# Kernel tuning notes

Hardware: AMD Instinct MI355X
Metric: run time of the kernel (lower is better)

## Reference

```python
import jax, jax.numpy as jnp
import numpy as np

SEQ, B, XD = 2048, 4, 16
D, NH, DFF, L, M = 256, 8, 512, 2, 1024
DH = D // NH
NEG_INF = -1e9  # finite stand-in for -inf (same softmax result, grad-safe)


def setup_inputs() -> dict:
    key = jax.random.key(0)
    ks = iter(jax.random.split(key, 40))

    def w(shape, s=0.02):
        return jax.random.normal(next(ks), shape, dtype=jnp.float32) * s

    return {
        "x": jax.random.normal(next(ks), (SEQ, B, XD), dtype=jnp.float32),
        "y": jax.random.normal(next(ks), (SEQ, B), dtype=jnp.float32),
        "single_eval_pos": M,
        "xenc_w": w((D, XD)), "xenc_b": w((D,)),
        "yenc_w": w((D, 1)), "yenc_b": w((D,)),
        "in_proj_w": w((L, 3 * D, D)), "in_proj_b": w((L, 3 * D)),
        "out_proj_w": w((L, D, D)), "out_proj_b": w((L, D)),
        "ln1_g": jnp.ones((L, D), jnp.float32), "ln1_b": jnp.zeros((L, D), jnp.float32),
        "lin1_w": w((L, DFF, D)), "lin1_b": w((L, DFF)),
        "lin2_w": w((L, D, DFF)), "lin2_b": w((L, D)),
        "ln2_g": jnp.ones((L, D), jnp.float32), "ln2_b": jnp.zeros((L, D), jnp.float32),
        "head_w1": w((DFF, D)), "head_b1": w((DFF,)),
        "head_w2": w((1, DFF)), "head_b2": w((1,)),
    }


def _layer_norm(x, g, b, eps=1e-5):
    mu = jnp.mean(x, axis=-1, keepdims=True)
    var = jnp.var(x, axis=-1, keepdims=True)
    return (x - mu) * jax.lax.rsqrt(var + eps) * g + b


def _forward(x, y, M_, p):
    seq, batch = y.shape
    x_src = x @ p["xenc_w"].T + p["xenc_b"]                     # [seq, b, D]
    y_src = y[..., None] @ p["yenc_w"].T + p["yenc_b"]           # [seq, b, D]
    tokens = jnp.concatenate([x_src[:M_] + y_src[:M_], x_src[M_:]], axis=0)

    # prefix-block + diagonal mask: keep (j < M) or (i == j)
    i = jnp.arange(seq)
    keep = (i[None, :] < M_) | (i[:, None] == i[None, :])
    mask = jnp.where(keep, 0.0, NEG_INF).astype(tokens.dtype)    # [seq, seq]

    h = tokens
    for l in range(p["in_proj_w"].shape[0]):
        qkv = h @ p["in_proj_w"][l].T + p["in_proj_b"][l]        # [seq, b, 3D]
        q, k, v = jnp.split(qkv, 3, axis=-1)
        to_heads = lambda t: t.reshape(seq, batch, NH, DH).transpose(1, 2, 0, 3)
        q, k, v = to_heads(q), to_heads(k), to_heads(v)          # [b, h, s, dh]
        scores = jnp.einsum("bhqd,bhkd->bhqk", q, k) / np.float32(np.sqrt(DH)) + mask
        attn = jax.nn.softmax(scores, axis=-1)
        o = jnp.einsum("bhqk,bhkd->bhqd", attn, v)
        o = o.transpose(2, 0, 1, 3).reshape(seq, batch, D)
        o = o @ p["out_proj_w"][l].T + p["out_proj_b"][l]
        h = _layer_norm(h + o, p["ln1_g"][l], p["ln1_b"][l])      # post-norm
        ff = jax.nn.gelu(h @ p["lin1_w"][l].T + p["lin1_b"][l], approximate=False)
        ff = ff @ p["lin2_w"][l].T + p["lin2_b"][l]
        h = _layer_norm(h + ff, p["ln2_g"][l], p["ln2_b"][l])

    q_out = h[M_:]                                               # [seq-M, b, D]
    hid = jax.nn.gelu(q_out @ p["head_w1"].T + p["head_b1"], approximate=False)
    return hid @ p["head_w2"].T + p["head_b2"]                   # [seq-M, b, 1]


def reference(x, y, single_eval_pos, xenc_w, xenc_b, yenc_w, yenc_b,
              in_proj_w, in_proj_b, out_proj_w, out_proj_b,
              ln1_g, ln1_b, lin1_w, lin1_b, lin2_w, lin2_b, ln2_g, ln2_b,
              head_w1, head_b1, head_w2, head_b2):
    p = dict(xenc_w=xenc_w, xenc_b=xenc_b, yenc_w=yenc_w, yenc_b=yenc_b,
             in_proj_w=in_proj_w, in_proj_b=in_proj_b,
             out_proj_w=out_proj_w, out_proj_b=out_proj_b,
             ln1_g=ln1_g, ln1_b=ln1_b, lin1_w=lin1_w, lin1_b=lin1_b,
             lin2_w=lin2_w, lin2_b=lin2_b, ln2_g=ln2_g, ln2_b=ln2_b,
             head_w1=head_w1, head_b1=head_b1, head_w2=head_w2, head_b2=head_b2)
    return _forward(x, y, int(single_eval_pos), p)
```

## Files before the change

kernel.cpp:

```cpp
#include <hip/hip_runtime.h>
#include <hip/hip_bf16.h>
#include <math.h>

#define SEQ    2048
#define BATCH  4
#define XDIM   16
#define DMODEL 256
#define NHEAD  8
#define DH     32
#define DFF    512
#define NLAYER 2
#define MPOS   1024
#define ROWS   (SEQ*BATCH)

#define ATT_SCALE 0.17677669529663687f

typedef __attribute__((ext_vector_type(8))) short bf16x8;
typedef __attribute__((ext_vector_type(4))) float f32x4;

__device__ __forceinline__ float gelu_exact(float x) {
    return 0.5f * x * (1.0f + erff(x * 0.70710678118654752f));
}
__device__ __forceinline__ short f2bf(float f) {
    unsigned int u = __float_as_uint(f);
    u += 0x7FFFu + ((u >> 16) & 1u);
    return (short)(u >> 16);
}
__device__ __forceinline__ float bf2f(unsigned short u) {
    return __uint_as_float(((unsigned int)u) << 16);
}
__device__ __forceinline__ void gload16(const unsigned short* g, unsigned short* l) {
    __builtin_amdgcn_global_load_lds(
        (const __attribute__((address_space(1))) unsigned int*)g,
        (__attribute__((address_space(3))) unsigned int*)l, 16, 0, 0);
}
#define VMWAIT(N) asm volatile("s_waitcnt vmcnt(" #N ")" ::: "memory")
__device__ __forceinline__ void pipe_barrier() {
    __builtin_amdgcn_sched_barrier(0);
    __builtin_amdgcn_s_barrier();
    __builtin_amdgcn_sched_barrier(0);
}

__global__ __launch_bounds__(256) void encode_cast(
    const float* __restrict__ x, const float* __restrict__ y,
    const float* __restrict__ xw, const float* __restrict__ xb,
    const float* __restrict__ yw, const float* __restrict__ yb,
    float* __restrict__ h, unsigned short* __restrict__ hb,
    const float* __restrict__ s0, const float* __restrict__ s1,
    const float* __restrict__ s2, const float* __restrict__ s3,
    const float* __restrict__ s4,
    unsigned short* __restrict__ d0, unsigned short* __restrict__ d1,
    unsigned short* __restrict__ d2, unsigned short* __restrict__ d3,
    unsigned short* __restrict__ d4)
{
    if (blockIdx.x < ROWS/4) {
        int g = blockIdx.x;
        int d = threadIdx.x;
        __shared__ float xs[4][XDIM];
        __shared__ float ys[4];
        if (d < 64) xs[d>>4][d&15] = x[(size_t)(g*4 + (d>>4))*XDIM + (d&15)];
        if (d < 4)  ys[d] = y[g*4 + d];
        __syncthreads();
        float wreg[XDIM];
        #pragma unroll
        for (int k = 0; k < XDIM; ++k) wreg[k] = xw[d*XDIM + k];
        const float xbv = xb[d], ywv = yw[d], ybv = yb[d];
        const bool train = (g < MPOS);
        #pragma unroll
        for (int r = 0; r < 4; ++r) {
            int row = g*4 + r;
            float acc = xbv;
            #pragma unroll
            for (int k = 0; k < XDIM; ++k) acc = fmaf(xs[r][k], wreg[k], acc);
            if (train) acc += ys[r]*ywv + ybv;
            h[(size_t)row*DMODEL + d]  = acc;
            hb[(size_t)row*DMODEL + d] = (unsigned short)f2bf(acc);
        }
        return;
    }
    int i = (blockIdx.x - ROWS/4)*256 + threadIdx.x;
    if (i >= 147456) return;
    const float* s; unsigned short* d; int off;
    if      (i <  49152) { s = s0; d = d0; off = i; }
    else if (i <  65536) { s = s1; d = d1; off = i - 49152; }
    else if (i <  98304) { s = s2; d = d2; off = i - 65536; }
    else if (i < 131072) { s = s3; d = d3; off = i - 98304; }
    else                 { s = s4; d = d4; off = i - 131072; }
    float4 a = *(const float4*)(s + (size_t)off*8);
    float4 c = *(const float4*)(s + (size_t)off*8 + 4);
    ushort4 u0, u1;
    u0.x=(unsigned short)f2bf(a.x); u0.y=(unsigned short)f2bf(a.y);
    u0.z=(unsigned short)f2bf(a.z); u0.w=(unsigned short)f2bf(a.w);
    u1.x=(unsigned short)f2bf(c.x); u1.y=(unsigned short)f2bf(c.y);
    u1.z=(unsigned short)f2bf(c.z); u1.w=(unsigned short)f2bf(c.w);
    *(ushort4*)(d + (size_t)off*8)     = u0;
    *(ushort4*)(d + (size_t)off*8 + 4) = u1;
}

__global__ __launch_bounds__(256) void gemm_qkv(
    const unsigned short* __restrict__ A, const unsigned short* __restrict__ B,
    const float* __restrict__ bias,
    unsigned short* __restrict__ Qg, unsigned short* __restrict__ Kg,
    unsigned short* __restrict__ Vg, int K)
{
    __shared__ unsigned short As[2][128][64];
    __shared__ unsigned short Bs[2][64][64];
    int tid  = threadIdx.x;
    int w    = tid >> 6, lane = tid & 63;
    int col  = lane & 15, quad = lane >> 4;
    int u    = blockIdx.x >> 3, xcd = blockIdx.x & 7;
    int by   = xcd*8 + u/12, bx = u%12;
    int m0   = by * 128, n0 = bx * 64;
    int l8   = lane >> 3;
    int c8s  = (((lane & 7) ^ l8) * 8);

    f32x4 acc[2][4];
    #pragma unroll
    for (int i = 0; i < 2; ++i)
        #pragma unroll
        for (int j = 0; j < 4; ++j) acc[i][j] = (f32x4){0.f,0.f,0.f,0.f};

    const unsigned short* ga = A + (size_t)(m0 + w*32 + l8)*K + c8s;
    const unsigned short* gb = B + (size_t)(n0 + w*16 + l8)*K + c8s;
    const int NS = K / 64;

    #pragma unroll
    for (int t = 0; t < 4; ++t) gload16(ga + (size_t)(t*8)*K, &As[0][w*32 + t*8][0]);
    #pragma unroll
    for (int t = 0; t < 2; ++t) gload16(gb + (size_t)(t*8)*K, &Bs[0][w*16 + t*8][0]);

    for (int s = 0; s < NS; ++s) {
        VMWAIT(0);
        pipe_barrier();
        if (s + 1 < NS) {
            int k2 = (s + 1) * 64;
            int nb = (s + 1) & 1;
            #pragma unroll
            for (int t = 0; t < 4; ++t) gload16(ga + k2 + (size_t)(t*8)*K, &As[nb][w*32 + t*8][0]);
            #pragma unroll
            for (int t = 0; t < 2; ++t) gload16(gb + k2 + (size_t)(t*8)*K, &Bs[nb][w*16 + t*8][0]);
        }
        int cur = s & 1;
        #pragma unroll
        for (int kk = 0; kk < 2; ++kk) {
            const int so = (((kk*4 + quad) ^ (col & 7)) * 8);
            bf16x8 af[2], bfr[4];
            #pragma unroll
            for (int i = 0; i < 2; ++i) af[i]  = *(const bf16x8*)&As[cur][w*32 + i*16 + col][so];
            #pragma unroll
            for (int j = 0; j < 4; ++j) bfr[j] = *(const bf16x8*)&Bs[cur][j*16 + col][so];
            #pragma unroll
            for (int i = 0; i < 2; ++i)
                #pragma unroll
                for (int j = 0; j < 4; ++j)
                    acc[i][j] = __builtin_amdgcn_mfma_f32_16x16x32_bf16(bfr[j], af[i], acc[i][j], 0, 0, 0);
        }
    }

    int region = n0 >> 8;
    if (region < 2) {
        #pragma unroll
        for (int i = 0; i < 2; ++i) {
            int m = m0 + w*32 + i*16 + col;
            int s = m >> 2, bidx = m & 3;
            #pragma unroll
            for (int j = 0; j < 4; ++j) {
                int ng = n0 + j*16 + quad*4;
                float4 bi = *(const float4*)&bias[ng];
                ushort4 uu;
                uu.x=(unsigned short)f2bf(acc[i][j][0] + bi.x);
                uu.y=(unsigned short)f2bf(acc[i][j][1] + bi.y);
                uu.z=(unsigned short)f2bf(acc[i][j][2] + bi.z);
                uu.w=(unsigned short)f2bf(acc[i][j][3] + bi.w);
                int np = ng - (region << 8);
                int hh = np >> 5, d = np & 31;
                int bh = bidx*NHEAD + hh;
                if (region == 0)
                    *(ushort4*)(Qg + ((size_t)(bh*SEQ + s))*DH + d) = uu;
                else
                    *(ushort4*)(Kg + ((size_t)(bh*SEQ + s))*DH + d) = uu;
            }
        }
    } else {
        __syncthreads();
        unsigned short* T3 = (unsigned short*)As;
        #pragma unroll
        for (int i = 0; i < 2; ++i) {
            int mi = w*32 + i*16 + col;
            int ss = mi >> 2, bidx = mi & 3;
            #pragma unroll
            for (int j = 0; j < 4; ++j) {
                int ni = j*16 + quad*4;
                float4 bi = *(const float4*)&bias[n0 + ni];
                T3[((ni    )*4 + bidx)*32 + ss] = (unsigned short)f2bf(acc[i][j][0] + bi.x);
                T3[((ni + 1)*4 + bidx)*32 + ss] = (unsigned short)f2bf(acc[i][j][1] + bi.y);
                T3[((ni + 2)*4 + bidx)*32 + ss] = (unsigned short)f2bf(acc[i][j][2] + bi.z);
                T3[((ni + 3)*4 + bidx)*32 + ss] = (unsigned short)f2bf(acc[i][j][3] + bi.w);
            }
        }
        __syncthreads();
        int sBase = m0 >> 2;
        #pragma unroll
        for (int r = 0; r < 4; ++r) {
            int chunk = tid + 256*r;
            int l = chunk >> 2, p = chunk & 3;
            int d = l & 31, hh_l = (l >> 5) & 1, bidx = l >> 6;
            int ni = hh_l*32 + d;
            int hh = ((n0 & 255) + ni) >> 5;
            int bh = bidx*NHEAD + hh;
            uint4 val = *(const uint4*)&T3[(ni*4 + bidx)*32 + p*8];
            *(uint4*)(Vg + ((size_t)(bh*DH + d))*SEQ + sBase + p*8) = val;
        }
    }
}

__global__ __launch_bounds__(256) void attn_mfma(
    const unsigned short* __restrict__ Qg,
    const unsigned short* __restrict__ Kg,
    const unsigned short* __restrict__ Vg,
    unsigned short* __restrict__ o)
{
    const int id  = blockIdx.x;
    const int sl  = id >> 3;
    const int bh  = (id & 7) * 4 + (sl >> 4);
    const int qt2 = sl & 15;
    const int h   = bh & 7;
    const int b   = bh >> 3;
    const int q0A = qt2 * 64;
    const int q0B = MPOS + qt2 * 64;
    const int tid  = threadIdx.x;
    const int w    = tid >> 6;
    const int lane = tid & 63;
    const int col  = lane & 15;
    const int quad = lane >> 4;

    __shared__ unsigned short Kt[2][128][40];
    __shared__ unsigned short Vt[2][32][136];
    __shared__ unsigned short PtA[4][16][136];
    __shared__ unsigned short PtB[4][16][136];

    const int qA = q0A + 16*w + col;
    const int qB = q0B + 16*w + col;
    bf16x8 qfA = *(const bf16x8*)(Qg + ((size_t)(bh*SEQ + qA))*DH + quad*8);
    bf16x8 qfB = *(const bf16x8*)(Qg + ((size_t)(bh*SEQ + qB))*DH + quad*8);

    f32x4 O0A = {0.f,0.f,0.f,0.f}, O1A = {0.f,0.f,0.f,0.f};
    f32x4 O0B = {0.f,0.f,0.f,0.f}, O1B = {0.f,0.f,0.f,0.f};
    float lsumA = 0.f, lsumB = 0.f;

    const int kRow = tid >> 2, kCh = (tid & 3) * 8;
    const int vD   = tid >> 3, vCh = (tid & 7) * 8;

    uint4 kreg0 = *(const uint4*)(Kg + ((size_t)(bh*SEQ + kRow     ))*DH + kCh);
    uint4 kreg1 = *(const uint4*)(Kg + ((size_t)(bh*SEQ + kRow + 64))*DH + kCh);
    uint4 vreg0 = *(const uint4*)(Vg + ((size_t)(bh*DH + vD))*SEQ + vCh);
    uint4 vreg1 = *(const uint4*)(Vg + ((size_t)(bh*DH + vD))*SEQ + vCh + 64);

    for (int kt = 0; kt < 8; ++kt) {
        const int p = kt & 1;
        *(uint4*)&Kt[p][kRow     ][kCh] = kreg0;
        *(uint4*)&Kt[p][kRow + 64][kCh] = kreg1;
        *(uint4*)&Vt[p][vD][vCh     ]   = vreg0;
        *(uint4*)&Vt[p][vD][vCh + 64]   = vreg1;
        __syncthreads();
        if (kt < 7) {
            int kn = (kt + 1) * 128;
            kreg0 = *(const uint4*)(Kg + ((size_t)(bh*SEQ + kn + kRow     ))*DH + kCh);
            kreg1 = *(const uint4*)(Kg + ((size_t)(bh*SEQ + kn + kRow + 64))*DH + kCh);
            vreg0 = *(const uint4*)(Vg + ((size_t)(bh*DH + vD))*SEQ + kn + vCh);
            vreg1 = *(const uint4*)(Vg + ((size_t)(bh*DH + vD))*SEQ + kn + vCh + 64);
        } else {
            kreg0 = *(const uint4*)(Kg + ((size_t)(bh*SEQ + q0B + kRow))*DH + kCh);
            vreg0 = *(const uint4*)(Vg + ((size_t)(bh*DH + vD))*SEQ + q0B + vCh);
        }

        #pragma unroll
        for (int mt = 0; mt < 8; ++mt) {
            bf16x8 kf = *(const bf16x8*)&Kt[p][mt*16 + col][quad*8];
            f32x4 stA = {0.f,0.f,0.f,0.f};
            stA = __builtin_amdgcn_mfma_f32_16x16x32_bf16(kf, qfA, stA, 0, 0, 0);
            ushort4 pwA;
            #pragma unroll
            for (int i = 0; i < 4; ++i) {
                float pv = __expf(stA[i]*ATT_SCALE);
                unsigned short us = (unsigned short)f2bf(pv);
                ((unsigned short*)&pwA)[i] = us;
                lsumA += bf2f(us);
            }
            *(ushort4*)&PtA[w][col][mt*16 + quad*4] = pwA;

            f32x4 stB = {0.f,0.f,0.f,0.f};
            stB = __builtin_amdgcn_mfma_f32_16x16x32_bf16(kf, qfB, stB, 0, 0, 0);
            ushort4 pwB;
            #pragma unroll
            for (int i = 0; i < 4; ++i) {
                float pv = __expf(stB[i]*ATT_SCALE);
                unsigned short us = (unsigned short)f2bf(pv);
                ((unsigned short*)&pwB)[i] = us;
                lsumB += bf2f(us);
            }
            *(ushort4*)&PtB[w][col][mt*16 + quad*4] = pwB;
        }
        #pragma unroll
        for (int c = 0; c < 4; ++c) {
            bf16x8 v0 = *(const bf16x8*)&Vt[p][col     ][c*32 + quad*8];
            bf16x8 v1 = *(const bf16x8*)&Vt[p][col + 16][c*32 + quad*8];
            bf16x8 pfA = *(const bf16x8*)&PtA[w][col][c*32 + quad*8];
            O0A = __builtin_amdgcn_mfma_f32_16x16x32_bf16(v0, pfA, O0A, 0, 0, 0);
            O1A = __builtin_amdgcn_mfma_f32_16x16x32_bf16(v1, pfA, O1A, 0, 0, 0);
            bf16x8 pfB = *(const bf16x8*)&PtB[w][col][c*32 + quad*8];
            O0B = __builtin_amdgcn_mfma_f32_16x16x32_bf16(v0, pfB, O0B, 0, 0, 0);
            O1B = __builtin_amdgcn_mfma_f32_16x16x32_bf16(v1, pfB, O1B, 0, 0, 0);
        }
    }

    *(uint4*)&Kt[0][kRow][kCh] = kreg0;
    *(uint4*)&Vt[0][vD][vCh]   = vreg0;
    __syncthreads();
    #pragma unroll
    for (int mt = 0; mt < 4; ++mt) {
        bf16x8 kf = *(const bf16x8*)&Kt[0][mt*16 + col][quad*8];
        f32x4 stB = {0.f,0.f,0.f,0.f};
        stB = __builtin_amdgcn_mfma_f32_16x16x32_bf16(kf, qfB, stB, 0, 0, 0);
        ushort4 pwB;
        #pragma unroll
        for (int i = 0; i < 4; ++i) {
            float pv = __expf(stB[i]*ATT_SCALE);
            if (mt*16 + quad*4 + i != 16*w + col) pv = 0.f;
            unsigned short us = (unsigned short)f2bf(pv);
            ((unsigned short*)&pwB)[i] = us;
            lsumB += bf2f(us);
        }
        *(ushort4*)&PtB[w][col][mt*16 + quad*4] = pwB;
    }
    #pragma unroll
    for (int c = 0; c < 2; ++c) {
        bf16x8 v0 = *(const bf16x8*)&Vt[0][col     ][c*32 + quad*8];
        bf16x8 v1 = *(const bf16x8*)&Vt[0][col + 16][c*32 + quad*8];
        bf16x8 pfB = *(const bf16x8*)&PtB[w][col][c*32 + quad*8];
        O0B = __builtin_amdgcn_mfma_f32_16x16x32_bf16(v0, pfB, O0B, 0, 0, 0);
        O1B = __builtin_amdgcn_mfma_f32_16x16x32_bf16(v1, pfB, O1B, 0, 0, 0);
    }

    lsumA += __shfl_xor(lsumA, 16, 64); lsumA += __shfl_xor(lsumA, 32, 64);
    lsumB += __shfl_xor(lsumB, 16, 64); lsumB += __shfl_xor(lsumB, 32, 64);
    float invA = 1.0f / lsumA, invB = 1.0f / lsumB;
    ushort4 u0, u1;
    #pragma unroll
    for (int i = 0; i < 4; ++i) {
        ((unsigned short*)&u0)[i] = (unsigned short)f2bf(O0A[i]*invA);
        ((unsigned short*)&u1)[i] = (unsigned short)f2bf(O1A[i]*invA);
    }
    unsigned short* opA = o + ((size_t)(qA*BATCH + b))*DMODEL + h*DH;
    *(ushort4*)(opA + quad*4)      = u0;
    *(ushort4*)(opA + 16 + quad*4) = u1;
    #pragma unroll
    for (int i = 0; i < 4; ++i) {
        ((unsigned short*)&u0)[i] = (unsigned short)f2bf(O0B[i]*invB);
        ((unsigned short*)&u1)[i] = (unsigned short)f2bf(O1B[i]*invB);
    }
    unsigned short* opB = o + ((size_t)(qB*BATCH + b))*DMODEL + h*DH;
    *(ushort4*)(opB + quad*4)      = u0;
    *(ushort4*)(opB + 16 + quad*4) = u1;
}

__global__ __launch_bounds__(256) void mlp_fused(
    const unsigned short* __restrict__ attb,
    const unsigned short* __restrict__ Wout, const float* __restrict__ ob,
    const float* __restrict__ g1, const float* __restrict__ be1,
    const unsigned short* __restrict__ W1, const float* __restrict__ fb1,
    const unsigned short* __restrict__ W2, const float* __restrict__ fb2,
    const float* __restrict__ g2, const float* __restrict__ be2,
    float* __restrict__ h, unsigned short* __restrict__ hb,
    const unsigned short* __restrict__ Wh1, const float* __restrict__ hb1,
    const float* __restrict__ hw2, const float* __restrict__ hb2,
    float* __restrict__ out, int doHead)
{
    __shared__ unsigned short Bs[3][256][64];
    __shared__ __align__(16) unsigned char smem_u[33280];
    __shared__ unsigned short Ht[2][16][264];
    __shared__ float sP[2][4][16], qP[2][4][16];

    typedef unsigned short AsT[2][16][64];
    AsT* As = reinterpret_cast<AsT*>(smem_u);
    typedef unsigned short PtT[16][520];
    PtT* Pt = reinterpret_cast<PtT*>(smem_u);

    const int tid  = threadIdx.x;
    const int w    = tid >> 6;
    const int lane = tid & 63;
    const int col  = lane & 15;
    const int quad = lane >> 4;
    const int l8   = lane >> 3;
    const int c8s  = (((lane & 7) ^ l8) * 8);
    const int bid  = blockIdx.x;
    const int m0a  = bid * 16;
    const int m0b  = 4096 + bid * 16;
    const int ma   = m0a + col;
    const int mb   = m0b + col;

    float resid[2][4][4];

    {
        f32x4 acc[2][4];
        #pragma unroll
        for (int g = 0; g < 2; ++g)
            #pragma unroll
            for (int j = 0; j < 4; ++j) acc[g][j] = (f32x4){0.f,0.f,0.f,0.f};

        const int gr = w >> 1;
        const unsigned short* gaw = attb + (size_t)((gr ? m0b : m0a) + (w&1)*8 + l8)*DMODEL + c8s;
        const unsigned short* gb  = Wout + (size_t)(w*64 + l8)*DMODEL + c8s;
        const int NS = DMODEL / 64;

        #pragma unroll
        for (int pb = 0; pb < 2; ++pb) {
            int k = pb * 64;
            gload16(gaw + k, &As[pb][gr][(w&1)*8][0]);
            #pragma unroll
            for (int t = 0; t < 8; ++t)
                gload16(gb + k + (size_t)(t*8)*DMODEL, &Bs[pb][w*64 + t*8][0]);
        }
        int bcur = 0;
        for (int s = 0; s < NS; ++s) {
            if (s == NS - 1) { VMWAIT(0); } else { VMWAIT(9); }
            pipe_barrier();
            if (s + 2 < NS) {
                int bpre = bcur + 2; if (bpre >= 3) bpre -= 3;
                int k2 = (s + 2) * 64;
                gload16(gaw + k2, &As[bpre][gr][(w&1)*8][0]);
                #pragma unroll
                for (int t = 0; t < 8; ++t)
                    gload16(gb + k2 + (size_t)(t*8)*DMODEL, &Bs[bpre][w*64 + t*8][0]);
            }
            #pragma unroll
            for (int kk = 0; kk < 2; ++kk) {
                const int so = (((kk*4 + quad) ^ (col & 7)) * 8);
                bf16x8 af0 = *(const bf16x8*)&As[bcur][0][col][so];
                bf16x8 af1 = *(const bf16x8*)&As[bcur][1][col][so];
                #pragma unroll
                for (int j = 0; j < 4; ++j) {
                    bf16x8 bfr = *(const bf16x8*)&Bs[bcur][w*64 + j*16 + col][so];
                    acc[0][j] = __builtin_amdgcn_mfma_f32_16x16x32_bf16(bfr, af0, acc[0][j], 0, 0, 0);
                    acc[1][j] = __builtin_amdgcn_mfma_f32_16x16x32_bf16(bfr, af1, acc[1][j], 0, 0, 0);
                }
            }
            bcur = (bcur == 2) ? 0 : bcur + 1;
        }

        float ssum[2] = {0.f, 0.f}, qsum[2] = {0.f, 0.f};
        #pragma unroll
        for (int g = 0; g < 2; ++g) {
            int m = g ? mb : ma;
            #pragma unroll
            for (int j = 0; j < 4; ++j) {
                int n = w*64 + j*16 + quad*4;
                float4 bi = *(const float4*)&ob[n];
                float4 hv = *(const float4*)&h[(size_t)m*DMODEL + n];
                #pragma unroll
                for (int i = 0; i < 4; ++i) {
                    float val = acc[g][j][i] + ((const float*)&bi)[i] + ((const float*)&hv)[i];
                    resid[g][j][i] = val;
                    ssum[g] += val; qsum[g] += val*val;
                }
            }
        }
        #pragma unroll
        for (int g = 0; g < 2; ++g) {
            ssum[g] += __shfl_xor(ssum[g], 16, 64); ssum[g] += __shfl_xor(ssum[g], 32, 64);
            qsum[g] += __shfl_xor(qsum[g], 16, 64); qsum[g] += __shfl_xor(qsum[g], 32, 64);
        }
        if (quad == 0) {
            sP[0][w][col] = ssum[0]; qP[0][w][col] = qsum[0];
            sP[1][w][col] = ssum[1]; qP[1][w][col] = qsum[1];
        }
        __syncthreads();
        #pragma unroll
        for (int g = 0; g < 2; ++g) {
            float st = sP[g][0][col] + sP[g][1][col] + sP[g][2][col] + sP[g][3][col];
            float qt = qP[g][0][col] + qP[g][1][col] + qP[g][2][col] + qP[g][3][col];
            float mu   = st * (1.0f/DMODEL);
            float var  = qt * (1.0f/DMODEL) - mu*mu;
            float rstd = rsqrtf(var + 1e-5f);
            #pragma unroll
            for (int j = 0; j < 4; ++j) {
                int n = w*64 + j*16 + quad*4;
                float4 gv = *(const float4*)&g1[n];
                float4 bv = *(const float4*)&be1[n];
                ushort4 u;
                #pragma unroll
                for (int i = 0; i < 4; ++i) {
                    float o = (resid[g][j][i]-mu)*rstd*((const float*)&gv)[i] + ((const float*)&bv)[i];
                    resid[g][j][i] = o;
                    ((unsigned short*)&u)[i] = (unsigned short)f2bf(o);
                }
                *(ushort4*)&Ht[g][col][n] = u;
            }
        }
        __syncthreads();
    }

    #pragma unroll 1
    for (int nh = 0; nh < 2; ++nh) {
        f32x4 acc[2][4];
        #pragma unroll
        for (int g = 0; g < 2; ++g)
            #pragma unroll
            for (int j = 0; j < 4; ++j) acc[g][j] = (f32x4){0.f,0.f,0.f,0.f};
        const unsigned short* gb = W1 + (size_t)(nh*256 + w*64 + l8)*DMODEL + c8s;
        const int NS = DMODEL / 64;

        #pragma unroll
        for (int pb = 0; pb < 2; ++pb)
            #pragma unroll
            for (int t = 0; t < 8; ++t)
                gload16(gb + pb*64 + (size_t)(t*8)*DMODEL, &Bs[pb][w*64 + t*8][0]);

        int bcur = 0;
        for (int s = 0; s < NS; ++s) {
            if (s == NS - 1) { VMWAIT(0); } else { VMWAIT(8); }
            pipe_barrier();
            if (s + 2 < NS) {
                int bpre = bcur + 2; if (bpre >= 3) bpre -= 3;
                int k2 = (s + 2) * 64;
                #pragma unroll
                for (int t = 0; t < 8; ++t)
                    gload16(gb + k2 + (size_t)(t*8)*DMODEL, &Bs[bpre][w*64 + t*8][0]);
            }
            #pragma unroll
            for (int kk = 0; kk < 2; ++kk) {
                const int so = (((kk*4 + quad) ^ (col & 7)) * 8);
                bf16x8 af0 = *(const bf16x8*)&Ht[0][col][s*64 + kk*32 + quad*8];
                bf16x8 af1 = *(const bf16x8*)&Ht[1][col][s*64 + kk*32 + quad*8];
                #pragma unroll
                for (int j = 0; j < 4; ++j) {
                    bf16x8 bfr = *(const bf16x8*)&Bs[bcur][w*64 + j*16 + col][so];
                    acc[0][j] = __builtin_amdgcn_mfma_f32_16x16x32_bf16(bfr, af0, acc[0][j], 0, 0, 0);
                    acc[1][j] = __builtin_amdgcn_mfma_f32_16x16x32_bf16(bfr, af1, acc[1][j], 0, 0, 0);
                }
            }
            bcur = (bcur == 2) ? 0 : bcur + 1;
        }
        #pragma unroll
        for (int g = 0; g < 2; ++g)
            #pragma unroll
            for (int j = 0; j < 4; ++j) {
                int n2 = nh*256 + w*64 + j*16 + quad*4;
                float4 bi = *(const float4*)&fb1[n2];
                ushort4 u;
                #pragma unroll
                for (int i = 0; i < 4; ++i)
                    ((unsigned short*)&u)[i] = (unsigned short)f2bf(gelu_exact(acc[g][j][i] + ((const float*)&bi)[i]));
                *(ushort4*)&Pt[g][col][n2] = u;
            }
        pipe_barrier();
    }

    {
        __syncthreads();
        f32x4 acc[2][4];
        #pragma unroll
        for (int g = 0; g < 2; ++g)
            #pragma unroll
            for (int j = 0; j < 4; ++j) acc[g][j] = (f32x4){0.f,0.f,0.f,0.f};
        const unsigned short* gb = W2 + (size_t)(w*64 + l8)*DFF + c8s;
        const int NS = DFF / 64;

        #pragma unroll
        for (int pb = 0; pb < 2; ++pb)
            #pragma unroll
            for (int t = 0; t < 8; ++t)
                gload16(gb + pb*64 + (size_t)(t*8)*DFF, &Bs[pb][w*64 + t*8][0]);

        int bcur = 0;
        for (int s = 0; s < NS; ++s) {
            if (s == NS - 1) { VMWAIT(0); } else { VMWAIT(8); }
            pipe_barrier();
            if (s + 2 < NS) {
                int bpre = bcur + 2; if (bpre >= 3) bpre -= 3;
                int k2 = (s + 2) * 64;
                #pragma unroll
                for (int t = 0; t < 8; ++t)
                    gload16(gb + k2 + (size_t)(t*8)*DFF, &Bs[bpre][w*64 + t*8][0]);
            }
            #pragma unroll
            for (int kk = 0; kk < 2; ++kk) {
                const int so = (((kk*4 + quad) ^ (col & 7)) * 8);
                bf16x8 af0 = *(const bf16x8*)&Pt[0][col][s*64 + kk*32 + quad*8];
                bf16x8 af1 = *(const bf16x8*)&Pt[1][col][s*64 + kk*32 + quad*8];
                #pragma unroll
                for (int j = 0; j < 4; ++j) {
                    bf16x8 bfr = *(const bf16x8*)&Bs[bcur][w*64 + j*16 + col][so];
                    acc[0][j] = __builtin_amdgcn_mfma_f32_16x16x32_bf16(bfr, af0, acc[0][j], 0, 0, 0);
                    acc[1][j] = __builtin_amdgcn_mfma_f32_16x16x32_bf16(bfr, af1, acc[1][j], 0, 0, 0);
                }
            }
            bcur = (bcur == 2) ? 0 : bcur + 1;
        }

        float ssum[2] = {0.f, 0.f}, qsum[2] = {0.f, 0.f};
        #pragma unroll
        for (int g = 0; g < 2; ++g)
            #pragma unroll
            for (int j = 0; j < 4; ++j) {
                int n = w*64 + j*16 + quad*4;
                float4 bi = *(const float4*)&fb2[n];
                #pragma unroll
                for (int i = 0; i < 4; ++i) {
                    float val = acc[g][j][i] + ((const float*)&bi)[i] + resid[g][j][i];
                    resid[g][j][i] = val;
                    ssum[g] += val; qsum[g] += val*val;
                }
            }
        #pragma unroll
        for (int g = 0; g < 2; ++g) {
            ssum[g] += __shfl_xor(ssum[g], 16, 64); ssum[g] += __shfl_xor(ssum[g], 32, 64);
            qsum[g] += __shfl_xor(qsum[g], 16, 64); qsum[g] += __shfl_xor(qsum[g], 32, 64);
        }
        if (quad == 0) {
            sP[0][w][col] = ssum[0]; qP[0][w][col] = qsum[0];
            sP[1][w][col] = ssum[1]; qP[1][w][col] = qsum[1];
        }
        __syncthreads();
        #pragma unroll
        for (int g = 0; g < 2; ++g) {
            int m = g ? mb : ma;
            float st = sP[g][0][col] + sP[g][1][col] + sP[g][2][col] + sP[g][3][col];
            float qt = qP[g][0][col] + qP[g][1][col] + qP[g][2][col] + qP[g][3][col];
            float mu   = st * (1.0f/DMODEL);
            float var  = qt * (1.0f/DMODEL) - mu*mu;
            float rstd = rsqrtf(var + 1e-5f);
            #pragma unroll
            for (int j = 0; j < 4; ++j) {
                int n = w*64 + j*16 + quad*4;
                float4 gv = *(const float4*)&g2[n];
                float4 bv = *(const float4*)&be2[n];
                float4 o;
                ushort4 u;
                #pragma unroll
                for (int i = 0; i < 4; ++i) {
                    float ov = (resid[g][j][i]-mu)*rstd*((const float*)&gv)[i] + ((const float*)&bv)[i];
                    ((float*)&o)[i] = ov;
                    ((unsigned short*)&u)[i] = (unsigned short)f2bf(ov);
                }
                *(float4*)&h[(size_t)m*DMODEL + n] = o;
                *(ushort4*)(hb + (size_t)m*DMODEL + n) = u;
                *(ushort4*)&Ht[g][col][n] = u;
            }
        }
        __syncthreads();
    }

    if (doHead) {
        float sdot = 0.f;
        #pragma unroll 1
        for (int nh = 0; nh < 2; ++nh) {
            f32x4 acc[4];
            #pragma unroll
            for (int j = 0; j < 4; ++j) acc[j] = (f32x4){0.f,0.f,0.f,0.f};
            const unsigned short* gb = Wh1 + (size_t)(nh*256 + w*64 + l8)*DMODEL + c8s;
            const int NS = DMODEL / 64;

            #pragma unroll
            for (int pb = 0; pb < 2; ++pb)
                #pragma unroll
                for (int t = 0; t < 8; ++t)
                    gload16(gb + pb*64 + (size_t)(t*8)*DMODEL, &Bs[pb][w*64 + t*8][0]);

            int bcur = 0;
            for (int s = 0; s < NS; ++s) {
                if (s == NS - 1) { VMWAIT(0); } else { VMWAIT(8); }
                pipe_barrier();
                if (s + 2 < NS) {
                    int bpre = bcur + 2; if (bpre >= 3) bpre -= 3;
                    int k2 = (s + 2) * 64;
                    #pragma unroll
                    for (int t = 0; t < 8; ++t)
                        gload16(gb + k2 + (size_t)(t*8)*DMODEL, &Bs[bpre][w*64 + t*8][0]);
                }
                #pragma unroll
                for (int kk = 0; kk < 2; ++kk) {
                    const int so = (((kk*4 + quad) ^ (col & 7)) * 8);
                    bf16x8 af = *(const bf16x8*)&Ht[1][col][s*64 + kk*32 + quad*8];
                    #pragma unroll
                    for (int j = 0; j < 4; ++j) {
                        bf16x8 bfr = *(const bf16x8*)&Bs[bcur][w*64 + j*16 + col][so];
                        acc[j] = __builtin_amdgcn_mfma_f32_16x16x32_bf16(bfr, af, acc[j], 0, 0, 0);
                    }
                }
                bcur = (bcur == 2) ? 0 : bcur + 1;
            }
            #pragma unroll
            for (int j = 0; j < 4; ++j) {
                int n2 = nh*256 + w*64 + j*16 + quad*4;
                float4 b1v = *(const float4*)&hb1[n2];
                float4 w2v = *(const float4*)&hw2[n2];
                #pragma unroll
                for (int i = 0; i < 4; ++i)
                    sdot += gelu_exact(acc[j][i] + ((const float*)&b1v)[i]) * ((const float*)&w2v)[i];
            }
            pipe_barrier();
        }
        sdot += __shfl_xor(sdot, 16, 64); sdot += __shfl_xor(sdot, 32, 64);
        if (quad == 0) sP[0][w][col] = sdot;
        __syncthreads();
        if (tid < 16)
            out[bid*16 + tid] = sP[0][0][tid] + sP[0][1][tid] + sP[0][2][tid] + sP[0][3][tid] + hb2[0];
    }
}

extern "C" void kernel_launch(void* const* d_in, const int* in_sizes, int n_in,
                              void* d_out, int out_size, void* d_ws, size_t ws_size,
                              hipStream_t stream)
{
    const float* x        = (const float*)d_in[0];
    const float* y        = (const float*)d_in[1];
    const float* xenc_w   = (const float*)d_in[3];
    const float* xenc_b   = (const float*)d_in[4];
    const float* yenc_w   = (const float*)d_in[5];
    const float* yenc_b   = (const float*)d_in[6];
    const float* in_proj_w  = (const float*)d_in[7];
    const float* in_proj_b  = (const float*)d_in[8];
    const float* out_proj_w = (const float*)d_in[9];
    const float* out_proj_b = (const float*)d_in[10];
    const float* ln1_g    = (const float*)d_in[11];
    const float* ln1_b    = (const float*)d_in[12];
    const float* lin1_w   = (const float*)d_in[13];
    const float* lin1_b   = (const float*)d_in[14];
    const float* lin2_w   = (const float*)d_in[15];
    const float* lin2_b   = (const float*)d_in[16];
    const float* ln2_g    = (const float*)d_in[17];
    const float* ln2_b    = (const float*)d_in[18];
    const float* head_w1  = (const float*)d_in[19];
    const float* head_b1  = (const float*)d_in[20];
    const float* head_w2  = (const float*)d_in[21];
    const float* head_b2  = (const float*)d_in[22];
    float* out = (float*)d_out;

    float* ws  = (float*)d_ws;
    float* h    = ws;
    unsigned short* hb    = (unsigned short*)(h + (size_t)ROWS*DMODEL);
    unsigned short* attb  = hb    + (size_t)ROWS*DMODEL;
    unsigned short* Qg    = attb  + (size_t)ROWS*DMODEL;
    unsigned short* Kg    = Qg    + (size_t)BATCH*NHEAD*SEQ*DH;
    unsigned short* Vg    = Kg    + (size_t)BATCH*NHEAD*SEQ*DH;
    unsigned short* Wqkv  = Vg    + (size_t)BATCH*NHEAD*SEQ*DH;
    unsigned short* Wout  = Wqkv  + (size_t)NLAYER*3*DMODEL*DMODEL;
    unsigned short* Wl1   = Wout  + (size_t)NLAYER*DMODEL*DMODEL;
    unsigned short* Wl2   = Wl1   + (size_t)NLAYER*DFF*DMODEL;
    unsigned short* Wh1   = Wl2   + (size_t)NLAYER*DMODEL*DFF;

    encode_cast<<<ROWS/4 + 576, 256, 0, stream>>>(
        x, y, xenc_w, xenc_b, yenc_w, yenc_b, h, hb,
        in_proj_w, out_proj_w, lin1_w, lin2_w, head_w1,
        Wqkv, Wout, Wl1, Wl2, Wh1);

    for (int l = 0; l < NLAYER; ++l) {
        gemm_qkv<<<768, 256, 0, stream>>>(
            hb, Wqkv + (size_t)l*3*DMODEL*DMODEL, in_proj_b + l*3*DMODEL,
            Qg, Kg, Vg, DMODEL);
        attn_mfma<<<512, 256, 0, stream>>>(Qg, Kg, Vg, attb);
        mlp_fused<<<256, 256, 0, stream>>>(
            attb,
            Wout + (size_t)l*DMODEL*DMODEL, out_proj_b + l*DMODEL,
            ln1_g + l*DMODEL, ln1_b + l*DMODEL,
            Wl1 + (size_t)l*DFF*DMODEL, lin1_b + l*DFF,
            Wl2 + (size_t)l*DMODEL*DFF, lin2_b + l*DMODEL,
            ln2_g + l*DMODEL, ln2_b + l*DMODEL,
            h, hb,
            Wh1, head_b1, head_w2, head_b2,
            out, (l == NLAYER-1) ? 1 : 0);
    }
}
```

Before: 236.4 us.

## Double query tiles per attention block and prefetch next MLP weight tiles early

The attention kernel now handles four 64-query tiles per block (two prefix, two query) instead of two, halving the grid to 256 blocks. Each K/V tile staged in shared memory is reused across twice as many queries, and the diagonal tail now loads a full 128-key block. In the fused MLP kernel, the first weight tiles for the next GEMM stage are issued right after the previous stage's main loop, before its epilogue, so the loads overlap the LayerNorm and GELU epilogues. In exchange, the attention kernel uses more shared memory and registers and runs with fewer blocks, which may lower occupancy and leave CUs idle on a large GPU.

```diff
diff --git a/kernel.cpp b/kernel.cpp
--- a/kernel.cpp
+++ b/kernel.cpp
@@ -222,12 +222,11 @@
 {
     const int id  = blockIdx.x;
     const int sl  = id >> 3;
-    const int bh  = (id & 7) * 4 + (sl >> 4);
-    const int qt2 = sl & 15;
+    const int bh  = (id & 7) * 4 + (sl >> 3);
+    const int qt4 = sl & 7;
     const int h   = bh & 7;
     const int b   = bh >> 3;
-    const int q0A = qt2 * 64;
-    const int q0B = MPOS + qt2 * 64;
+    const int q0  = qt4 * 128;
     const int tid  = threadIdx.x;
     const int w    = tid >> 6;
     const int lane = tid & 63;
@@ -236,17 +235,25 @@
 
     __shared__ unsigned short Kt[2][128][40];
     __shared__ unsigned short Vt[2][32][136];
-    __shared__ unsigned short PtA[4][16][136];
-    __shared__ unsigned short PtB[4][16][136];
-
-    const int qA = q0A + 16*w + col;
-    const int qB = q0B + 16*w + col;
-    bf16x8 qfA = *(const bf16x8*)(Qg + ((size_t)(bh*SEQ + qA))*DH + quad*8);
-    bf16x8 qfB = *(const bf16x8*)(Qg + ((size_t)(bh*SEQ + qB))*DH + quad*8);
-
-    f32x4 O0A = {0.f,0.f,0.f,0.f}, O1A = {0.f,0.f,0.f,0.f};
-    f32x4 O0B = {0.f,0.f,0.f,0.f}, O1B = {0.f,0.f,0.f,0.f};
-    float lsumA = 0.f, lsumB = 0.f;
+    __shared__ unsigned short PtA0[4][16][136];
+    __shared__ unsigned short PtA1[4][16][136];
+    __shared__ unsigned short PtB0[4][16][136];
+    __shared__ unsigned short PtB1[4][16][136];
+
+    const int qA0 = q0 + 16*w + col;
+    const int qA1 = q0 + 64 + 16*w + col;
+    const int qB0 = MPOS + q0 + 16*w + col;
+    const int qB1 = MPOS + q0 + 64 + 16*w + col;
+    bf16x8 qfA0 = *(const bf16x8*)(Qg + ((size_t)(bh*SEQ + qA0))*DH + quad*8);
+    bf16x8 qfA1 = *(const bf16x8*)(Qg + ((size_t)(bh*SEQ + qA1))*DH + quad*8);
+    bf16x8 qfB0 = *(const bf16x8*)(Qg + ((size_t)(bh*SEQ + qB0))*DH + quad*8);
+    bf16x8 qfB1 = *(const bf16x8*)(Qg + ((size_t)(bh*SEQ + qB1))*DH + quad*8);
+
+    f32x4 O0A0 = {0.f,0.f,0.f,0.f}, O1A0 = {0.f,0.f,0.f,0.f};
+    f32x4 O0A1 = {0.f,0.f,0.f,0.f}, O1A1 = {0.f,0.f,0.f,0.f};
+    f32x4 O0B0 = {0.f,0.f,0.f,0.f}, O1B0 = {0.f,0.f,0.f,0.f};
+    f32x4 O0B1 = {0.f,0.f,0.f,0.f}, O1B1 = {0.f,0.f,0.f,0.f};
+    float lsumA0 = 0.f, lsumA1 = 0.f, lsumB0 = 0.f, lsumB1 = 0.f;
 
     const int kRow = tid >> 2, kCh = (tid & 3) * 8;
     const int vD   = tid >> 3, vCh = (tid & 7) * 8;
@@ -263,105 +270,162 @@
         *(uint4*)&Vt[p][vD][vCh     ]   = vreg0;
         *(uint4*)&Vt[p][vD][vCh + 64]   = vreg1;
         __syncthreads();
-        if (kt < 7) {
-            int kn = (kt + 1) * 128;
+        {
+            int kn = (kt < 7) ? (kt + 1) * 128 : (MPOS + q0);
             kreg0 = *(const uint4*)(Kg + ((size_t)(bh*SEQ + kn + kRow     ))*DH + kCh);
             kreg1 = *(const uint4*)(Kg + ((size_t)(bh*SEQ + kn + kRow + 64))*DH + kCh);
             vreg0 = *(const uint4*)(Vg + ((size_t)(bh*DH + vD))*SEQ + kn + vCh);
             vreg1 = *(const uint4*)(Vg + ((size_t)(bh*DH + vD))*SEQ + kn + vCh + 64);
-        } else {
-            kreg0 = *(const uint4*)(Kg + ((size_t)(bh*SEQ + q0B + kRow))*DH + kCh);
-            vreg0 = *(const uint4*)(Vg + ((size_t)(bh*DH + vD))*SEQ + q0B + vCh);
         }
 
         #pragma unroll
         for (int mt = 0; mt < 8; ++mt) {
             bf16x8 kf = *(const bf16x8*)&Kt[p][mt*16 + col][quad*8];
-            f32x4 stA = {0.f,0.f,0.f,0.f};
-            stA = __builtin_amdgcn_mfma_f32_16x16x32_bf16(kf, qfA, stA, 0, 0, 0);
-            ushort4 pwA;
+            f32x4 st; ushort4 pw;
+
+            st = (f32x4){0.f,0.f,0.f,0.f};
+            st = __builtin_amdgcn_mfma_f32_16x16x32_bf16(kf, qfA0, st, 0, 0, 0);
             #pragma unroll
             for (int i = 0; i < 4; ++i) {
-                float pv = __expf(stA[i]*ATT_SCALE);
-                unsigned short us = (unsigned short)f2bf(pv);
-                ((unsigned short*)&pwA)[i] = us;
-                lsumA += bf2f(us);
-            }
-            *(ushort4*)&PtA[w][col][mt*16 + quad*4] = pwA;
-
-            f32x4 stB = {0.f,0.f,0.f,0.f};
-            stB = __builtin_amdgcn_mfma_f32_16x16x32_bf16(kf, qfB, stB, 0, 0, 0);
-            ushort4 pwB;
+                unsigned short us = (unsigned short)f2bf(__expf(st[i]*ATT_SCALE));
+                ((unsigned short*)&pw)[i] = us; lsumA0 += bf2f(us);
+            }
+            *(ushort4*)&PtA0[w][col][mt*16 + quad*4] = pw;
+
+            st = (f32x4){0.f,0.f,0.f,0.f};
+            st = __builtin_amdgcn_mfma_f32_16x16x32_bf16(kf, qfA1, st, 0, 0, 0);
             #pragma unroll
             for (int i = 0; i < 4; ++i) {
-                float pv = __expf(stB[i]*ATT_SCALE);
-                unsigned short us = (unsigned short)f2bf(pv);
-                ((unsigned short*)&pwB)[i] = us;
-                lsumB += bf2f(us);
-            }
-            *(ushort4*)&PtB[w][col][mt*16 + quad*4] = pwB;
+                unsigned short us = (unsigned short)f2bf(__expf(st[i]*ATT_SCALE));
+                ((unsigned short*)&pw)[i] = us; lsumA1 += bf2f(us);
+            }
+            *(ushort4*)&PtA1[w][col][mt*16 + quad*4] = pw;
+
+            st = (f32x4){0.f,0.f,0.f,0.f};
+            st = __builtin_amdgcn_mfma_f32_16x16x32_bf16(kf, qfB0, st, 0, 0, 0);
+            #pragma unroll
+            for (int i = 0; i < 4; ++i) {
+                unsigned short us = (unsigned short)f2bf(__expf(st[i]*ATT_SCALE));
+                ((unsigned short*)&pw)[i] = us; lsumB0 += bf2f(us);
+            }
+            *(ushort4*)&PtB0[w][col][mt*16 + quad*4] = pw;
+
+            st = (f32x4){0.f,0.f,0.f,0.f};
+            st = __builtin_amdgcn_mfma_f32_16x16x32_bf16(kf, qfB1, st, 0, 0, 0);
+            #pragma unroll
+            for (int i = 0; i < 4; ++i) {
+                unsigned short us = (unsigned short)f2bf(__expf(st[i]*ATT_SCALE));
+                ((unsigned short*)&pw)[i] = us; lsumB1 += bf2f(us);
+            }
+            *(ushort4*)&PtB1[w][col][mt*16 + quad*4] = pw;
         }
         #pragma unroll
         for (int c = 0; c < 4; ++c) {
             bf16x8 v0 = *(const bf16x8*)&Vt[p][col     ][c*32 + quad*8];
             bf16x8 v1 = *(const bf16x8*)&Vt[p][col + 16][c*32 + quad*8];
-            bf16x8 pfA = *(const bf16x8*)&PtA[w][col][c*32 + quad*8];
-            O0A = __builtin_amdgcn_mfma_f32_16x16x32_bf16(v0, pfA, O0A, 0, 0, 0);
-            O1A = __builtin_amdgcn_mfma_f32_16x16x32_bf16(v1, pfA, O1A, 0, 0, 0);
-            bf16x8 pfB = *(const bf16x8*)&PtB[w][col][c*32 + quad*8];
-            O0B = __builtin_amdgcn_mfma_f32_16x16x32_bf16(v0, pfB, O0B, 0, 0, 0);
-            O1B = __builtin_amdgcn_mfma_f32_16x16x32_bf16(v1, pfB, O1B, 0, 0, 0);
-        }
-    }
-
-    *(uint4*)&Kt[0][kRow][kCh] = kreg0;
-    *(uint4*)&Vt[0][vD][vCh]   = vreg0;
+            bf16x8 pf;
+            pf = *(const bf16x8*)&PtA0[w][col][c*32 + quad*8];
+            O0A0 = __builtin_amdgcn_mfma_f32_16x16x32_bf16(v0, pf, O0A0, 0, 0, 0);
+            O1A0 = __builtin_amdgcn_mfma_f32_16x16x32_bf16(v1, pf, O1A0, 0, 0, 0);
+            pf = *(const bf16x8*)&PtA1[w][col][c*32 + quad*8];
+            O0A1 = __builtin_amdgcn_mfma_f32_16x16x32_bf16(v0, pf, O0A1, 0, 0, 0);
+            O1A1 = __builtin_amdgcn_mfma_f32_16x16x32_bf16(v1, pf, O1A1, 0, 0, 0);
+            pf = *(const bf16x8*)&PtB0[w][col][c*32 + quad*8];
+            O0B0 = __builtin_amdgcn_mfma_f32_16x16x32_bf16(v0, pf, O0B0, 0, 0, 0);
+            O1B0 = __builtin_amdgcn_mfma_f32_16x16x32_bf16(v1, pf, O1B0, 0, 0, 0);
+            pf = *(const bf16x8*)&PtB1[w][col][c*32 + quad*8];
+            O0B1 = __builtin_amdgcn_mfma_f32_16x16x32_bf16(v0, pf, O0B1, 0, 0, 0);
+            O1B1 = __builtin_amdgcn_mfma_f32_16x16x32_bf16(v1, pf, O1B1, 0, 0, 0);
+        }
+    }
+
+    *(uint4*)&Kt[0][kRow     ][kCh] = kreg0;
+    *(uint4*)&Kt[0][kRow + 64][kCh] = kreg1;
+    *(uint4*)&Vt[0][vD][vCh     ]   = vreg0;
+    *(uint4*)&Vt[0][vD][vCh + 64]   = vreg1;
     __syncthreads();
     #pragma unroll
     for (int mt = 0; mt < 4; ++mt) {
         bf16x8 kf = *(const bf16x8*)&Kt[0][mt*16 + col][quad*8];
-        f32x4 stB = {0.f,0.f,0.f,0.f};
-        stB = __builtin_amdgcn_mfma_f32_16x16x32_bf16(kf, qfB, stB, 0, 0, 0);
-        ushort4 pwB;
+        f32x4 st = {0.f,0.f,0.f,0.f};
+        st = __builtin_amdgcn_mfma_f32_16x16x32_bf16(kf, qfB0, st, 0, 0, 0);
+        ushort4 pw;
         #pragma unroll
         for (int i = 0; i < 4; ++i) {
-            float pv = __expf(stB[i]*ATT_SCALE);
+            float pv = __expf(st[i]*ATT_SCALE);
             if (mt*16 + quad*4 + i != 16*w + col) pv = 0.f;
             unsigned short us = (unsigned short)f2bf(pv);
-            ((unsigned short*)&pwB)[i] = us;
-            lsumB += bf2f(us);
-        }
-        *(ushort4*)&PtB[w][col][mt*16 + quad*4] = pwB;
+            ((unsigned short*)&pw)[i] = us; lsumB0 += bf2f(us);
+        }
+        *(ushort4*)&PtB0[w][col][mt*16 + quad*4] = pw;
+    }
+    #pragma unroll
+    for (int mt = 4; mt < 8; ++mt) {
+        bf16x8 kf = *(const bf16x8*)&Kt[0][mt*16 + col][quad*8];
+        f32x4 st = {0.f,0.f,0.f,0.f};
+        st = __builtin_amdgcn_mfma_f32_16x16x32_bf16(kf, qfB1, st, 0, 0, 0);
+        ushort4 pw;
+        #pragma unroll
+        for (int i = 0; i < 4; ++i) {
+            float pv = __expf(st[i]*ATT_SCALE);
+            if (mt*16 + quad*4 + i - 64 != 16*w + col) pv = 0.f;
+            unsigned short us = (unsigned short)f2bf(pv);
+            ((unsigned short*)&pw)[i] = us; lsumB1 += bf2f(us);
+        }
+        *(ushort4*)&PtB1[w][col][(mt-4)*16 + quad*4] = pw;
     }
     #pragma unroll
     for (int c = 0; c < 2; ++c) {
         bf16x8 v0 = *(const bf16x8*)&Vt[0][col     ][c*32 + quad*8];
         bf16x8 v1 = *(const bf16x8*)&Vt[0][col + 16][c*32 + quad*8];
-        bf16x8 pfB = *(const bf16x8*)&PtB[w][col][c*32 + quad*8];
-        O0B = __builtin_amdgcn_mfma_f32_16x16x32_bf16(v0, pfB, O0B, 0, 0, 0);
-        O1B = __builtin_amdgcn_mfma_f32_16x16x32_bf16(v1, pfB, O1B, 0, 0, 0);
-    }
-
-    lsumA += __shfl_xor(lsumA, 16, 64); lsumA += __shfl_xor(lsumA, 32, 64);
-    lsumB += __shfl_xor(lsumB, 16, 64); lsumB += __shfl_xor(lsumB, 32, 64);
-    float invA = 1.0f / lsumA, invB = 1.0f / lsumB;
+        bf16x8 pf = *(const bf16x8*)&PtB0[w][col][c*32 + quad*8];
+        O0B0 = __builtin_amdgcn_mfma_f32_16x16x32_bf16(v0, pf, O0B0, 0, 0, 0);
+        O1B0 = __builtin_amdgcn_mfma_f32_16x16x32_bf16(v1, pf, O1B0, 0, 0, 0);
+    }
+    #pragma unroll
+    for (int c = 0; c < 2; ++c) {
+        bf16x8 v0 = *(const bf16x8*)&Vt[0][col     ][(c+2)*32 + quad*8];
+        bf16x8 v1 = *(const bf16x8*)&Vt[0][col + 16][(c+2)*32 + quad*8];
+        bf16x8 pf = *(const bf16x8*)&PtB1[w][col][c*32 + quad*8];
+        O0B1 = __builtin_amdgcn_mfma_f32_16x16x32_bf16(v0, pf, O0B1, 0, 0, 0);
+        O1B1 = __builtin_amdgcn_mfma_f32_16x16x32_bf16(v1, pf, O1B1, 0, 0, 0);
+    }
+
+    lsumA0 += __shfl_xor(lsumA0, 16, 64); lsumA0 += __shfl_xor(lsumA0, 32, 64);
+    lsumA1 += __shfl_xor(lsumA1, 16, 64); lsumA1 += __shfl_xor(lsumA1, 32, 64);
+    lsumB0 += __shfl_xor(lsumB0, 16, 64); lsumB0 += __shfl_xor(lsumB0, 32, 64);
+    lsumB1 += __shfl_xor(lsumB1, 16, 64); lsumB1 += __shfl_xor(lsumB1, 32, 64);
+    float invA0 = 1.0f / lsumA0, invA1 = 1.0f / lsumA1;
+    float invB0 = 1.0f / lsumB0, invB1 = 1.0f / lsumB1;
     ushort4 u0, u1;
     #pragma unroll
     for (int i = 0; i < 4; ++i) {
-        ((unsigned short*)&u0)[i] = (unsigned short)f2bf(O0A[i]*invA);
-        ((unsigned short*)&u1)[i] = (unsigned short)f2bf(O1A[i]*invA);
-    }
-    unsigned short* opA = o + ((size_t)(qA*BATCH + b))*DMODEL + h*DH;
-    *(ushort4*)(opA + quad*4)      = u0;
-    *(ushort4*)(opA + 16 + quad*4) = u1;
+        ((unsigned short*)&u0)[i] = (unsigned short)f2bf(O0A0[i]*invA0);
+        ((unsigned short*)&u1)[i] = (unsigned short)f2bf(O1A0[i]*invA0);
+    }
+    unsigned short* op = o + ((size_t)(qA0*BATCH + b))*DMODEL + h*DH;
+    *(ushort4*)(op + quad*4) = u0; *(ushort4*)(op + 16 + quad*4) = u1;
     #pragma unroll
     for (int i = 0; i < 4; ++i) {
-        ((unsigned short*)&u0)[i] = (unsigned short)f2bf(O0B[i]*invB);
-        ((unsigned short*)&u1)[i] = (unsigned short)f2bf(O1B[i]*invB);
-    }
-    unsigned short* opB = o + ((size_t)(qB*BATCH + b))*DMODEL + h*DH;
-    *(ushort4*)(opB + quad*4)      = u0;
-    *(ushort4*)(opB + 16 + quad*4) = u1;
+        ((unsigned short*)&u0)[i] = (unsigned short)f2bf(O0A1[i]*invA1);
+        ((unsigned short*)&u1)[i] = (unsigned short)f2bf(O1A1[i]*invA1);
+    }
+    op = o + ((size_t)(qA1*BATCH + b))*DMODEL + h*DH;
+    *(ushort4*)(op + quad*4) = u0; *(ushort4*)(op + 16 + quad*4) = u1;
+    #pragma unroll
+    for (int i = 0; i < 4; ++i) {
+        ((unsigned short*)&u0)[i] = (unsigned short)f2bf(O0B0[i]*invB0);
+        ((unsigned short*)&u1)[i] = (unsigned short)f2bf(O1B0[i]*invB0);
+    }
+    op = o + ((size_t)(qB0*BATCH + b))*DMODEL + h*DH;
+    *(ushort4*)(op + quad*4) = u0; *(ushort4*)(op + 16 + quad*4) = u1;
+    #pragma unroll
+    for (int i = 0; i < 4; ++i) {
+        ((unsigned short*)&u0)[i] = (unsigned short)f2bf(O0B1[i]*invB1);
+        ((unsigned short*)&u1)[i] = (unsigned short)f2bf(O1B1[i]*invB1);
+    }
+    op = o + ((size_t)(qB1*BATCH + b))*DMODEL + h*DH;
+    *(ushort4*)(op + quad*4) = u0; *(ushort4*)(op + 16 + quad*4) = u1;
 }
 
 __global__ __launch_bounds__(256) void mlp_fused(
@@ -447,24 +511,39 @@
             }
             bcur = (bcur == 2) ? 0 : bcur + 1;
         }
-
-        float ssum[2] = {0.f, 0.f}, qsum[2] = {0.f, 0.f};
+        pipe_barrier();
+
+        float4 hv[2][4];
         #pragma unroll
         for (int g = 0; g < 2; ++g) {
             int m = g ? mb : ma;
+            #pragma unroll
+            for (int j = 0; j < 4; ++j)
+                hv[g][j] = *(const float4*)&h[(size_t)m*DMODEL + w*64 + j*16 + quad*4];
+        }
+        {
+            const unsigned short* gbB = W1 + (size_t)(w*64 + l8)*DMODEL + c8s;
+            #pragma unroll
+            for (int pb = 0; pb < 2; ++pb)
+                #pragma unroll
+                for (int t = 0; t < 8; ++t)
+                    gload16(gbB + pb*64 + (size_t)(t*8)*DMODEL, &Bs[pb][w*64 + t*8][0]);
+        }
+
+        float ssum[2] = {0.f, 0.f}, qsum[2] = {0.f, 0.f};
+        #pragma unroll
+        for (int g = 0; g < 2; ++g)
             #pragma unroll
             for (int j = 0; j < 4; ++j) {
                 int n = w*64 + j*16 + quad*4;
                 float4 bi = *(const float4*)&ob[n];
-                float4 hv = *(const float4*)&h[(size_t)m*DMODEL + n];
                 #pragma unroll
                 for (int i = 0; i < 4; ++i) {
-                    float val = acc[g][j][i] + ((const float*)&bi)[i] + ((const float*)&hv)[i];
+                    float val = acc[g][j][i] + ((const float*)&bi)[i] + ((const float*)&hv[g][j])[i];
                     resid[g][j][i] = val;
                     ssum[g] += val; qsum[g] += val*val;
                 }
             }
-        }
         #pragma unroll
         for (int g = 0; g < 2; ++g) {
             ssum[g] += __shfl_xor(ssum[g], 16, 64); ssum[g] += __shfl_xor(ssum[g], 32, 64);
@@ -509,13 +588,6 @@
             for (int j = 0; j < 4; ++j) acc[g][j] = (f32x4){0.f,0.f,0.f,0.f};
         const unsigned short* gb = W1 + (size_t)(nh*256 + w*64 + l8)*DMODEL + c8s;
         const int NS = DMODEL / 64;
-
-        #pragma unroll
-        for (int pb = 0; pb < 2; ++pb)
-            #pragma unroll
-            for (int t = 0; t < 8; ++t)
-                gload16(gb + pb*64 + (size_t)(t*8)*DMODEL, &Bs[pb][w*64 + t*8][0]);
-
         int bcur = 0;
         for (int s = 0; s < NS; ++s) {
             if (s == NS - 1) { VMWAIT(0); } else { VMWAIT(8); }
@@ -541,6 +613,22 @@
             }
             bcur = (bcur == 2) ? 0 : bcur + 1;
         }
+        pipe_barrier();
+        if (nh == 0) {
+            const unsigned short* gb2 = W1 + (size_t)(256 + w*64 + l8)*DMODEL + c8s;
+            #pragma unroll
+            for (int pb = 0; pb < 2; ++pb)
+                #pragma unroll
+                for (int t = 0; t < 8; ++t)
+                    gload16(gb2 + pb*64 + (size_t)(t*8)*DMODEL, &Bs[pb][w*64 + t*8][0]);
+        } else {
+            const unsigned short* gbC = W2 + (size_t)(w*64 + l8)*DFF + c8s;
+            #pragma unroll
+            for (int pb = 0; pb < 2; ++pb)
+                #pragma unroll
+                for (int t = 0; t < 8; ++t)
+                    gload16(gbC + pb*64 + (size_t)(t*8)*DFF, &Bs[pb][w*64 + t*8][0]);
+        }
         #pragma unroll
         for (int g = 0; g < 2; ++g)
             #pragma unroll
@@ -553,7 +641,6 @@
                     ((unsigned short*)&u)[i] = (unsigned short)f2bf(gelu_exact(acc[g][j][i] + ((const float*)&bi)[i]));
                 *(ushort4*)&Pt[g][col][n2] = u;
             }
-        pipe_barrier();
     }
 
     {
@@ -565,13 +652,6 @@
             for (int j = 0; j < 4; ++j) acc[g][j] = (f32x4){0.f,0.f,0.f,0.f};
         const unsigned short* gb = W2 + (size_t)(w*64 + l8)*DFF + c8s;
         const int NS = DFF / 64;
-
-        #pragma unroll
-        for (int pb = 0; pb < 2; ++pb)
-            #pragma unroll
-            for (int t = 0; t < 8; ++t)
-                gload16(gb + pb*64 + (size_t)(t*8)*DFF, &Bs[pb][w*64 + t*8][0]);
-
         int bcur = 0;
         for (int s = 0; s < NS; ++s) {
             if (s == NS - 1) { VMWAIT(0); } else { VMWAIT(8); }
@@ -759,7 +839,7 @@
         gemm_qkv<<<768, 256, 0, stream>>>(
             hb, Wqkv + (size_t)l*3*DMODEL*DMODEL, in_proj_b + l*3*DMODEL,
             Qg, Kg, Vg, DMODEL);
-        attn_mfma<<<512, 256, 0, stream>>>(Qg, Kg, Vg, attb);
+        attn_mfma<<<256, 256, 0, stream>>>(Qg, Kg, Vg, attb);
         mlp_fused<<<256, 256, 0, stream>>>(
             attb,
             Wout + (size_t)l*DMODEL*DMODEL, out_proj_b + l*DMODEL,
```

Result: slower. 249.6 us (+5.6%).
